# Performance work log

Hardware: AMD Instinct MI355X
Metric: run time of the kernel (lower is better)

Reference implementation:

```python
import jax, jax.numpy as jnp
import numpy as np

B, D, H, NL, NB = 131072, 64, 512, 3, 8
d = D // 2
EPS = 1e-5


def _mlp(x, W0, b0, Wh, bh, Wo, bo, act):
    # x: [B, d] -> [B, d]; hidden width H, NL hidden->hidden layers, linear output
    h = act(x @ W0 + b0)
    for i in range(Wh.shape[0]):
        h = act(h @ Wh[i] + bh[i])
    return h @ Wo + bo


def setup_inputs() -> dict:
    key = jax.random.key(0)
    ks = jax.random.split(key, 16)
    s = 0.05
    inp = {
        "y": jax.random.normal(ks[0], (B, D), dtype=jnp.float32),
        # s-network params, stacked over blocks
        "sW0": jax.random.normal(ks[1], (NB, d, H), dtype=jnp.float32) * s,
        "sb0": jnp.zeros((NB, H), jnp.float32),
        "sWh": jax.random.normal(ks[2], (NB, NL, H, H), dtype=jnp.float32) * s,
        "sbh": jnp.zeros((NB, NL, H), jnp.float32),
        "sWo": jax.random.normal(ks[3], (NB, H, d), dtype=jnp.float32) * s,
        "sbo": jnp.zeros((NB, d), jnp.float32),
        # t-network params
        "tW0": jax.random.normal(ks[4], (NB, d, H), dtype=jnp.float32) * s,
        "tb0": jnp.zeros((NB, H), jnp.float32),
        "tWh": jax.random.normal(ks[5], (NB, NL, H, H), dtype=jnp.float32) * s,
        "tbh": jnp.zeros((NB, NL, H), jnp.float32),
        "tWo": jax.random.normal(ks[6], (NB, H, d), dtype=jnp.float32) * s,
        "tbo": jnp.zeros((NB, d), jnp.float32),
        # BatchNorm flow params (log_gamma, beta init at 0 as in torch module)
        "bn_log_gamma": jnp.zeros((NB, D), jnp.float32),
        "bn_beta": jnp.zeros((NB, D), jnp.float32),
    }
    return inp


def reference(y, sW0, sb0, sWh, sbh, sWo, sbo,
              tW0, tb0, tWh, tbh, tWo, tbo,
              bn_log_gamma, bn_beta):
    act_s, act_t = jnp.tanh, jax.nn.relu
    log_det = jnp.zeros((y.shape[0], 1), y.dtype)
    for b in range(NB):
        # alternating slice/compliment: even blocks condition on first half
        if b % 2 == 0:
            ys, yc = y[:, :d], y[:, d:]
        else:
            ys, yc = y[:, d:], y[:, :d]
        s_out = _mlp(ys, sW0[b], sb0[b], sWh[b], sbh[b], sWo[b], sbo[b], act_s)
        t_out = _mlp(ys, tW0[b], tb0[b], tWh[b], tbh[b], tWo[b], tbo[b], act_t)
        zc = yc * jnp.exp(s_out) + t_out
        z = jnp.concatenate([ys, zc], axis=1) if b % 2 == 0 else jnp.concatenate([zc, ys], axis=1)
        log_det = log_det + jnp.sum(s_out, axis=1, keepdims=True)
        # Batch_Norm flow (training mode: batch stats, unbiased var like torch .var(0))
        mean = z.mean(axis=0)
        var = z.var(axis=0, ddof=1)
        x_hat = (z - mean) / jnp.sqrt(var + EPS)
        y = jnp.exp(bn_log_gamma[b]) * x_hat + bn_beta[b]
        log_det = log_det + jnp.sum(bn_log_gamma[b] - 0.5 * jnp.log(var + EPS))
    return y, log_det
```

## Files before the change

### kernel.cpp

```cpp
#include <hip/hip_runtime.h>

#define NBLK 8
#define BROWS 131072
#define HDIM 512
#define EPSV 1e-5f
#define WROWS 64

typedef __bf16 bf16x8 __attribute__((ext_vector_type(8)));
typedef __bf16 bf16x4 __attribute__((ext_vector_type(4)));
typedef float f32x4 __attribute__((ext_vector_type(4)));

#define PACK_NET 819200
#define PACK_H 16384
#define PACK_HEAD 802816

__device__ __forceinline__ float act_tanh_f(float x) {
  float e = __expf(x + x);
  return fmaf(-2.f, __builtin_amdgcn_rcpf(e + 1.f), 1.f);
}

template <int ACT>
__device__ __forceinline__ float apply_act(float v) {
  if (ACT == 1) return act_tanh_f(v);
  return fmaxf(v, 0.f);
}

template <int ACT>
__device__ __forceinline__ void dense_hidden(const __bf16* __restrict__ Wp,
                                             const float* __restrict__ bias,
                                             __bf16* hb, int w, int c,
                                             int quad, int lane) {
  f32x4 acc[4][4];
#pragma unroll
  for (int rb = 0; rb < 4; ++rb)
#pragma unroll
    for (int ft = 0; ft < 4; ++ft) acc[rb][ft] = (f32x4){0.f, 0.f, 0.f, 0.f};
  const __bf16* wp = Wp + (size_t)(w * 2) * 16384 + lane * 8;
  bf16x8 br[3][4];
#pragma unroll
  for (int s = 0; s < 2; ++s)
#pragma unroll
    for (int ft = 0; ft < 4; ++ft)
      br[s][ft] = *(const bf16x8*)(wp + (ft >> 1) * 16384 + (ft & 1) * 512 +
                                   s * 1024);
  const int msk = (c & 7) << 3;
  __builtin_amdgcn_s_setprio(1);
#pragma unroll
  for (int kt = 0; kt < 16; ++kt) {
    if (kt + 2 < 16) {
#pragma unroll
      for (int ft = 0; ft < 4; ++ft)
        br[(kt + 2) % 3][ft] = *(const bf16x8*)(wp + (ft >> 1) * 16384 +
                                                (ft & 1) * 512 + (kt + 2) * 1024);
    }
    const int sk = (kt * 32 + quad * 8) ^ msk;
#pragma unroll
    for (int rb = 0; rb < 4; ++rb) {
      bf16x8 hv = *(const bf16x8*)&hb[(rb * 16 + c) * HDIM + sk];
#pragma unroll
      for (int ft = 0; ft < 4; ++ft)
        acc[rb][ft] = __builtin_amdgcn_mfma_f32_16x16x32_bf16(br[kt % 3][ft], hv, acc[rb][ft], 0, 0, 0);
    }
  }
  __builtin_amdgcn_s_setprio(0);
  __syncthreads();
#pragma unroll
  for (int ft = 0; ft < 4; ++ft) {
    const f32x4 bi = *(const f32x4*)&bias[w * 64 + ft * 16 + quad * 4];
    const int fsw = (w * 64 + ft * 16 + quad * 4) ^ msk;
#pragma unroll
    for (int rb = 0; rb < 4; ++rb) {
      bf16x4 pk;
#pragma unroll
      for (int i = 0; i < 4; ++i)
        pk[i] = (__bf16)apply_act<ACT>(acc[rb][ft][i] + bi[i]);
      *(bf16x4*)&hb[(rb * 16 + c) * HDIM + fsw] = pk;
    }
  }
  __syncthreads();
}

template <int ACT>
__device__ __forceinline__ void dense_l0(const __bf16* __restrict__ pw,
                                         const float* __restrict__ b0,
                                         const __bf16* __restrict__ ys,
                                         __bf16* hb, int w, int c, int quad,
                                         int lane) {
  bf16x8 aw[4];
#pragma unroll
  for (int ft = 0; ft < 4; ++ft)
    aw[ft] = *(const bf16x8*)&pw[(size_t)(w * 2 + (ft >> 1)) * 1024 +
                                 (ft & 1) * 512 + lane * 8];
  f32x4 acc[4][4];
#pragma unroll
  for (int rb = 0; rb < 4; ++rb)
#pragma unroll
    for (int ft = 0; ft < 4; ++ft) acc[rb][ft] = (f32x4){0.f, 0.f, 0.f, 0.f};
  const int ysk = (quad * 8) ^ ((c & 3) << 3);
  __builtin_amdgcn_s_setprio(1);
#pragma unroll
  for (int rb = 0; rb < 4; ++rb) {
    bf16x8 yb = *(const bf16x8*)&ys[(rb * 16 + c) * 32 + ysk];
#pragma unroll
    for (int ft = 0; ft < 4; ++ft)
      acc[rb][ft] = __builtin_amdgcn_mfma_f32_16x16x32_bf16(aw[ft], yb, acc[rb][ft], 0, 0, 0);
  }
  __builtin_amdgcn_s_setprio(0);
  const int msk = (c & 7) << 3;
#pragma unroll
  for (int ft = 0; ft < 4; ++ft) {
    const f32x4 bi = *(const f32x4*)&b0[w * 64 + ft * 16 + quad * 4];
    const int fsw = (w * 64 + ft * 16 + quad * 4) ^ msk;
#pragma unroll
    for (int rb = 0; rb < 4; ++rb) {
      bf16x4 pk;
#pragma unroll
      for (int i = 0; i < 4; ++i)
        pk[i] = (__bf16)apply_act<ACT>(acc[rb][ft][i] + bi[i]);
      *(bf16x4*)&hb[(rb * 16 + c) * HDIM + fsw] = pk;
    }
  }
}

__device__ __forceinline__ f32x4 dense_head(const __bf16* __restrict__ ph,
                                            const float* __restrict__ bo,
                                            const __bf16* __restrict__ hb,
                                            int fb, int rb, int c, int quad,
                                            int lane) {
  const __bf16* wp = ph + (size_t)fb * 8192 + lane * 8;
  bf16x8 hr[3];
  hr[0] = *(const bf16x8*)wp;
  hr[1] = *(const bf16x8*)(wp + 512);
  f32x4 acc = (f32x4){0.f, 0.f, 0.f, 0.f};
  const int msk = (c & 7) << 3;
  __builtin_amdgcn_s_setprio(1);
#pragma unroll
  for (int kt = 0; kt < 16; ++kt) {
    if (kt + 2 < 16) hr[(kt + 2) % 3] = *(const bf16x8*)(wp + (kt + 2) * 512);
    bf16x8 hv = *(const bf16x8*)&hb[(rb * 16 + c) * HDIM + ((kt * 32 + quad * 8) ^ msk)];
    acc = __builtin_amdgcn_mfma_f32_16x16x32_bf16(hr[kt % 3], hv, acc, 0, 0, 0);
  }
  __builtin_amdgcn_s_setprio(0);
  const int f0 = fb * 16 + quad * 4;
  f32x4 bo4 = *(const f32x4*)&bo[f0];
#pragma unroll
  for (int i = 0; i < 4; ++i) acc[i] += bo4[i];
  return acc;
}

template <bool FIRST>
__global__ __launch_bounds__(512, 4) void fused_block(
    const float* __restrict__ src, const __bf16* __restrict__ pwS,
    const __bf16* __restrict__ pwT, const float* __restrict__ sb0,
    const float* __restrict__ sbh, const float* __restrict__ sbo,
    const float* __restrict__ tb0, const float* __restrict__ tbh,
    const float* __restrict__ tbo, const float* __restrict__ prevP,
    float* __restrict__ zbuf, float* __restrict__ ld,
    float* __restrict__ stats_out, int o) {
  __shared__ __bf16 hbuf[WROWS * HDIM];
  __shared__ __bf16 ysb[WROWS * 32];
  __shared__ float tout[WROWS * 36];
  const int tid = threadIdx.x;
  const int w = tid >> 6, lane = tid & 63, c = lane & 15, quad = lane >> 4;
  const size_t row0 = (size_t)blockIdx.x * WROWS;

  {
    const int row = tid >> 3, sub = tid & 7;
    const int col0 = o + sub * 4;
    f32x4 yv = *(const f32x4*)&src[(row0 + row) * 64 + col0];
    bf16x4 pv;
#pragma unroll
    for (int j = 0; j < 4; ++j) {
      const float A_ = FIRST ? 1.f : prevP[col0 + j];
      const float C_ = FIRST ? 0.f : prevP[64 + col0 + j];
      pv[j] = (__bf16)fmaf(A_, yv[j], C_);
    }
    *(bf16x4*)&ysb[row * 32 + ((sub * 4) ^ ((row & 3) << 3))] = pv;
  }
  __syncthreads();

  const int fb = w & 1, rb = w >> 1;
  const int f0 = fb * 16 + quad * 4;
  const int r = rb * 16 + c;

  dense_l0<2>(pwT, tb0, ysb, hbuf, w, c, quad, lane);
  __syncthreads();
  dense_hidden<2>(pwT + PACK_H, tbh, hbuf, w, c, quad, lane);
  dense_hidden<2>(pwT + PACK_H + 262144, tbh + 512, hbuf, w, c, quad, lane);
  dense_hidden<2>(pwT + PACK_H + 2 * 262144, tbh + 1024, hbuf, w, c, quad, lane);
  {
    f32x4 tvh = dense_head(pwT + PACK_HEAD, tbo, hbuf, fb, rb, c, quad, lane);
    *(f32x4*)&tout[r * 36 + f0] = tvh;
  }
  __syncthreads();

  dense_l0<1>(pwS, sb0, ysb, hbuf, w, c, quad, lane);
  __syncthreads();
  dense_hidden<1>(pwS + PACK_H, sbh, hbuf, w, c, quad, lane);
  dense_hidden<1>(pwS + PACK_H + 262144, sbh + 512, hbuf, w, c, quad, lane);
  dense_hidden<1>(pwS + PACK_H + 2 * 262144, sbh + 1024, hbuf, w, c, quad, lane);
  f32x4 sacc = dense_head(pwS + PACK_HEAD, sbo, hbuf, fb, rb, c, quad, lane);
  float sv[4];
#pragma unroll
  for (int i = 0; i < 4; ++i) sv[i] = sacc[i];

  const size_t grow = row0 + r;
  f32x4 tv = *(const f32x4*)&tout[r * 36 + f0];
  __syncthreads();
  float* cs = (float*)hbuf;
  float* lda = cs + 128;
  if (tid < 128) cs[tid] = 0.f;
  else if (tid < 192) lda[tid - 128] = 0.f;
  __syncthreads();

  const int oc = o ^ 32;
  float zc[4], yn2[4];
  {
    f32x4 pA1, pC1, pA2, pC2;
    if (FIRST) {
      pA1 = pA2 = (f32x4){1.f, 1.f, 1.f, 1.f};
      pC1 = pC2 = (f32x4){0.f, 0.f, 0.f, 0.f};
    } else {
      pA1 = *(const f32x4*)&prevP[oc + f0];
      pC1 = *(const f32x4*)&prevP[64 + oc + f0];
      pA2 = *(const f32x4*)&prevP[o + f0];
      pC2 = *(const f32x4*)&prevP[64 + o + f0];
    }
    f32x4 yv = *(const f32x4*)&src[grow * 64 + oc + f0];
    f32x4 zo;
#pragma unroll
    for (int i = 0; i < 4; ++i) {
      zc[i] = fmaf(fmaf(pA1[i], yv[i], pC1[i]), __expf(sv[i]), tv[i]);
      zo[i] = zc[i];
    }
    *(f32x4*)&zbuf[grow * 64 + oc + f0] = zo;
    f32x4 yv2 = *(const f32x4*)&src[grow * 64 + o + f0];
    f32x4 yo;
#pragma unroll
    for (int i = 0; i < 4; ++i) {
      yn2[i] = fmaf(pA2[i], yv2[i], pC2[i]);
      yo[i] = yn2[i];
    }
    *(f32x4*)&zbuf[grow * 64 + o + f0] = yo;
  }

  {
    float ssum = sv[0] + sv[1] + sv[2] + sv[3];
    ssum += __shfl_xor(ssum, 16);
    ssum += __shfl_xor(ssum, 32);
    if (quad == 0) atomicAdd(&lda[r], ssum);
  }

#pragma unroll
  for (int i = 0; i < 4; ++i) {
    float v = zc[i], q = zc[i] * zc[i];
    float v2 = yn2[i], q2 = yn2[i] * yn2[i];
#pragma unroll
    for (int m = 1; m < 16; m <<= 1) {
      v += __shfl_xor(v, m);  q += __shfl_xor(q, m);
      v2 += __shfl_xor(v2, m); q2 += __shfl_xor(q2, m);
    }
    if (c == 0) {
      atomicAdd(&cs[oc + f0 + i], v);
      atomicAdd(&cs[64 + oc + f0 + i], q);
      atomicAdd(&cs[o + f0 + i], v2);
      atomicAdd(&cs[64 + o + f0 + i], q2);
    }
  }
  __syncthreads();
  if (tid < 128) {
    atomicAdd(&stats_out[tid], cs[tid]);
  } else if (tid < 192) {
    const int rr = tid - 128;
    const size_t gr = row0 + rr;
    if (FIRST) ld[gr] = lda[rr]; else ld[gr] += lda[rr];
  }
}


__global__ void stats_kernel(const float* __restrict__ raw,
                             const float* __restrict__ lg,
                             const float* __restrict__ beta,
                             float* __restrict__ param,
                             float* __restrict__ ld_scalar) {
  const int t = threadIdx.x;
  const float S = raw[t], SS = raw[64 + t];
  const float mean = S / (float)BROWS;
  const float var = (SS - S * mean) / (float)(BROWS - 1);
  const float inv = rsqrtf(var + EPSV);
  const float g = __expf(lg[t]);
  const float A = g * inv;
  param[t] = A;
  param[64 + t] = beta[t] - mean * A;
  float contrib = lg[t] - 0.5f * __logf(var + EPSV);
  contrib += __shfl_xor(contrib, 1);  contrib += __shfl_xor(contrib, 2);
  contrib += __shfl_xor(contrib, 4);  contrib += __shfl_xor(contrib, 8);
  contrib += __shfl_xor(contrib, 16); contrib += __shfl_xor(contrib, 32);
  if (t == 0) atomicAdd(ld_scalar, contrib);
}

__global__ void final_kernel(float* __restrict__ out,
                             const float* __restrict__ param7,
                             const float* __restrict__ ld_scalar) {
  const size_t gid = (size_t)blockIdx.x * 256 + threadIdx.x;
  const size_t total = (size_t)BROWS * 64;
  const int col = gid & 63;
  const float z = out[gid];
  out[gid] = param7[col] * z + param7[64 + col];
  if (gid < BROWS) out[total + gid] += ld_scalar[0];
}

__global__ void pack_weights(const float* __restrict__ sW0,
                             const float* __restrict__ sWh,
                             const float* __restrict__ sWo,
                             const float* __restrict__ tW0,
                             const float* __restrict__ tWh,
                             const float* __restrict__ tWo,
                             __bf16* __restrict__ dst) {
  const int gid = blockIdx.x * 256 + threadIdx.x;
  const int gpn = PACK_NET / 8;
  const int b = gid / (2 * gpn);
  const int rr0 = gid % (2 * gpn);
  const int net = rr0 / gpn;
  const size_t o = (size_t)(rr0 % gpn) * 8;
  const float* W0 = net ? tW0 : sW0;
  const float* Wh = net ? tWh : sWh;
  const float* Wo = net ? tWo : sWo;
  __bf16* d = dst + ((size_t)b * 2 + net) * PACK_NET + o;
  float v[8];
  if (o < PACK_H) {
    const int idx = (int)(o >> 3);
    const int lane = idx & 63, fbb = (idx >> 6) & 1, w = (idx >> 7) & 15;
    const int cc = lane & 15, q = lane >> 4;
    const int f = w * 32 + fbb * 16 + cc;
    const float* s = W0 + (size_t)b * 32 * 512;
#pragma unroll
    for (int j = 0; j < 8; ++j) v[j] = s[(size_t)(q * 8 + j) * 512 + f];
  } else if (o < PACK_HEAD) {
    const size_t oo = o - PACK_H;
    const int l = (int)(oo >> 18);
    const int idx = (int)((oo & 262143) >> 3);
    const int lane = idx & 63, fbb = (idx >> 6) & 1, kt = (idx >> 7) & 15,
              w = (idx >> 11) & 15;
    const int cc = lane & 15, q = lane >> 4;
    const int f = w * 32 + fbb * 16 + cc;
    const float* s = Wh + ((size_t)(b * 3 + l)) * 512 * 512;
#pragma unroll
    for (int j = 0; j < 8; ++j) v[j] = s[(size_t)(kt * 32 + q * 8 + j) * 512 + f];
  } else {
    const size_t oo = o - PACK_HEAD;
    const int idx = (int)(oo >> 3);
    const int lane = idx & 63, kt = (idx >> 6) & 15, fbb = (idx >> 10) & 1;
    const int cc = lane & 15, q = lane >> 4;
    const int f = fbb * 16 + cc;
    const float* s = Wo + (size_t)b * 512 * 32;
#pragma unroll
    for (int j = 0; j < 8; ++j) v[j] = s[(size_t)(kt * 32 + q * 8 + j) * 32 + f];
  }
  bf16x8 pv;
#pragma unroll
  for (int j = 0; j < 8; ++j) pv[j] = (__bf16)v[j];
  *(bf16x8*)d = pv;
}


extern "C" void kernel_launch(void* const* d_in, const int* in_sizes, int n_in,
                              void* d_out, int out_size, void* d_ws, size_t ws_size,
                              hipStream_t stream) {
  const float* y_in = (const float*)d_in[0];
  const float* sW0 = (const float*)d_in[1];
  const float* sb0 = (const float*)d_in[2];
  const float* sWh = (const float*)d_in[3];
  const float* sbh = (const float*)d_in[4];
  const float* sWo = (const float*)d_in[5];
  const float* sbo = (const float*)d_in[6];
  const float* tW0 = (const float*)d_in[7];
  const float* tb0 = (const float*)d_in[8];
  const float* tWh = (const float*)d_in[9];
  const float* tbh = (const float*)d_in[10];
  const float* tWo = (const float*)d_in[11];
  const float* tbo = (const float*)d_in[12];
  const float* bn_lg = (const float*)d_in[13];
  const float* bn_bt = (const float*)d_in[14];

  char* p = (char*)d_ws;
  __bf16* packed = (__bf16*)p; p += (size_t)NBLK * 2 * PACK_NET * 2;
  float* stats_raw = (float*)p; p += NBLK * 128 * 4;
  float* ld_scalar = (float*)p; p += 256;
  float* stats_param = (float*)p; p += NBLK * 128 * 4;

  float* out = (float*)d_out;
  float* zbuf = out;
  float* ld = out + (size_t)BROWS * 64;

  pack_weights<<<(NBLK * 2 * PACK_NET / 8) / 256, 256, 0, stream>>>(
      sW0, sWh, sWo, tW0, tWh, tWo, packed);
  hipMemsetAsync(stats_raw, 0, NBLK * 128 * 4 + 256, stream);

  const int GG = BROWS / WROWS;

  for (int b = 0; b < NBLK; ++b) {
    const int o = (b & 1) ? 32 : 0;
    const __bf16* pwS = packed + (size_t)b * 2 * PACK_NET;
    const __bf16* pwT = pwS + PACK_NET;
    float* praw = stats_raw + b * 128;
    const float* srcb = (b == 0) ? y_in : zbuf;

    if (b == 0) {
      fused_block<true><<<GG, 512, 0, stream>>>(srcb, pwS, pwT,
          sb0, sbh, sbo, tb0, tbh, tbo, nullptr, zbuf, ld, praw, o);
    } else {
      fused_block<false><<<GG, 512, 0, stream>>>(srcb, pwS, pwT,
          sb0 + b * 512, sbh + (size_t)b * 1536, sbo + b * 32,
          tb0 + b * 512, tbh + (size_t)b * 1536, tbo + b * 32,
          stats_param + (size_t)(b - 1) * 128, zbuf, ld, praw, o);
    }
    stats_kernel<<<1, 64, 0, stream>>>(praw, bn_lg + b * 64, bn_bt + b * 64,
                                       stats_param + (size_t)b * 128, ld_scalar);
  }

  final_kernel<<<(BROWS * 64) / 256, 256, 0, stream>>>(
      out, stats_param + 7 * 128, ld_scalar);
}
```

Before: 3.913 ms.

## Reorder hidden weight pack k-major and alternate s/t net order per block

Measured after the change: 3.991 ms. No clear change (+2.0%).

```diff
diff --git a/kernel.cpp b/kernel.cpp
--- a/kernel.cpp
+++ b/kernel.cpp
@@ -19,44 +19,37 @@
   return fmaf(-2.f, __builtin_amdgcn_rcpf(e + 1.f), 1.f);
 }
 
-template <int ACT>
-__device__ __forceinline__ float apply_act(float v) {
-  if (ACT == 1) return act_tanh_f(v);
-  return fmaxf(v, 0.f);
-}
-
-template <int ACT>
 __device__ __forceinline__ void dense_hidden(const __bf16* __restrict__ Wp,
                                              const float* __restrict__ bias,
-                                             __bf16* hb, int w, int c,
+                                             __bf16* hb, int act, int w, int c,
                                              int quad, int lane) {
   f32x4 acc[4][4];
 #pragma unroll
   for (int rb = 0; rb < 4; ++rb)
 #pragma unroll
     for (int ft = 0; ft < 4; ++ft) acc[rb][ft] = (f32x4){0.f, 0.f, 0.f, 0.f};
-  const __bf16* wp = Wp + (size_t)(w * 2) * 16384 + lane * 8;
+  const __bf16* wp = Wp + (size_t)w * 2048 + lane * 8;
   bf16x8 br[3][4];
 #pragma unroll
   for (int s = 0; s < 2; ++s)
 #pragma unroll
     for (int ft = 0; ft < 4; ++ft)
-      br[s][ft] = *(const bf16x8*)(wp + (ft >> 1) * 16384 + (ft & 1) * 512 +
-                                   s * 1024);
+      br[s][ft] = *(const bf16x8*)(wp + s * 16384 + ft * 512);
   const int msk = (c & 7) << 3;
+  const int rowb = c << 9;
+  const int qb = quad << 3;
   __builtin_amdgcn_s_setprio(1);
 #pragma unroll
   for (int kt = 0; kt < 16; ++kt) {
     if (kt + 2 < 16) {
 #pragma unroll
       for (int ft = 0; ft < 4; ++ft)
-        br[(kt + 2) % 3][ft] = *(const bf16x8*)(wp + (ft >> 1) * 16384 +
-                                                (ft & 1) * 512 + (kt + 2) * 1024);
-    }
-    const int sk = (kt * 32 + quad * 8) ^ msk;
+        br[(kt + 2) % 3][ft] = *(const bf16x8*)(wp + (kt + 2) * 16384 + ft * 512);
+    }
+    const int sk = (((kt * 32 + qb) ^ msk) + rowb);
 #pragma unroll
     for (int rb = 0; rb < 4; ++rb) {
-      bf16x8 hv = *(const bf16x8*)&hb[(rb * 16 + c) * HDIM + sk];
+      bf16x8 hv = *(const bf16x8*)&hb[sk + rb * 8192];
 #pragma unroll
       for (int ft = 0; ft < 4; ++ft)
         acc[rb][ft] = __builtin_amdgcn_mfma_f32_16x16x32_bf16(br[kt % 3][ft], hv, acc[rb][ft], 0, 0, 0);
@@ -64,33 +57,48 @@
   }
   __builtin_amdgcn_s_setprio(0);
   __syncthreads();
-#pragma unroll
-  for (int ft = 0; ft < 4; ++ft) {
-    const f32x4 bi = *(const f32x4*)&bias[w * 64 + ft * 16 + quad * 4];
-    const int fsw = (w * 64 + ft * 16 + quad * 4) ^ msk;
-#pragma unroll
-    for (int rb = 0; rb < 4; ++rb) {
-      bf16x4 pk;
-#pragma unroll
-      for (int i = 0; i < 4; ++i)
-        pk[i] = (__bf16)apply_act<ACT>(acc[rb][ft][i] + bi[i]);
-      *(bf16x4*)&hb[(rb * 16 + c) * HDIM + fsw] = pk;
-    }
-  }
-  __syncthreads();
-}
-
-template <int ACT>
+  const int wq = w * 64 + quad * 4;
+  if (act == 1) {
+#pragma unroll
+    for (int ft = 0; ft < 4; ++ft) {
+      const f32x4 bi = *(const f32x4*)&bias[wq + ft * 16];
+      const int fsw = ((wq + ft * 16) ^ msk) + rowb;
+#pragma unroll
+      for (int rb = 0; rb < 4; ++rb) {
+        bf16x4 pk;
+#pragma unroll
+        for (int i = 0; i < 4; ++i)
+          pk[i] = (__bf16)act_tanh_f(acc[rb][ft][i] + bi[i]);
+        *(bf16x4*)&hb[fsw + rb * 8192] = pk;
+      }
+    }
+  } else {
+#pragma unroll
+    for (int ft = 0; ft < 4; ++ft) {
+      const f32x4 bi = *(const f32x4*)&bias[wq + ft * 16];
+      const int fsw = ((wq + ft * 16) ^ msk) + rowb;
+#pragma unroll
+      for (int rb = 0; rb < 4; ++rb) {
+        bf16x4 pk;
+#pragma unroll
+        for (int i = 0; i < 4; ++i)
+          pk[i] = (__bf16)fmaxf(acc[rb][ft][i] + bi[i], 0.f);
+        *(bf16x4*)&hb[fsw + rb * 8192] = pk;
+      }
+    }
+  }
+  __syncthreads();
+}
+
 __device__ __forceinline__ void dense_l0(const __bf16* __restrict__ pw,
                                          const float* __restrict__ b0,
                                          const __bf16* __restrict__ ys,
-                                         __bf16* hb, int w, int c, int quad,
-                                         int lane) {
+                                         __bf16* hb, int act, int w, int c,
+                                         int quad, int lane) {
   bf16x8 aw[4];
 #pragma unroll
   for (int ft = 0; ft < 4; ++ft)
-    aw[ft] = *(const bf16x8*)&pw[(size_t)(w * 2 + (ft >> 1)) * 1024 +
-                                 (ft & 1) * 512 + lane * 8];
+    aw[ft] = *(const bf16x8*)&pw[(size_t)w * 2048 + ft * 512 + lane * 8];
   f32x4 acc[4][4];
 #pragma unroll
   for (int rb = 0; rb < 4; ++rb)
@@ -107,17 +115,35 @@
   }
   __builtin_amdgcn_s_setprio(0);
   const int msk = (c & 7) << 3;
-#pragma unroll
-  for (int ft = 0; ft < 4; ++ft) {
-    const f32x4 bi = *(const f32x4*)&b0[w * 64 + ft * 16 + quad * 4];
-    const int fsw = (w * 64 + ft * 16 + quad * 4) ^ msk;
-#pragma unroll
-    for (int rb = 0; rb < 4; ++rb) {
-      bf16x4 pk;
-#pragma unroll
-      for (int i = 0; i < 4; ++i)
-        pk[i] = (__bf16)apply_act<ACT>(acc[rb][ft][i] + bi[i]);
-      *(bf16x4*)&hb[(rb * 16 + c) * HDIM + fsw] = pk;
+  const int rowb = c << 9;
+  const int wq = w * 64 + quad * 4;
+  if (act == 1) {
+#pragma unroll
+    for (int ft = 0; ft < 4; ++ft) {
+      const f32x4 bi = *(const f32x4*)&b0[wq + ft * 16];
+      const int fsw = ((wq + ft * 16) ^ msk) + rowb;
+#pragma unroll
+      for (int rb = 0; rb < 4; ++rb) {
+        bf16x4 pk;
+#pragma unroll
+        for (int i = 0; i < 4; ++i)
+          pk[i] = (__bf16)act_tanh_f(acc[rb][ft][i] + bi[i]);
+        *(bf16x4*)&hb[fsw + rb * 8192] = pk;
+      }
+    }
+  } else {
+#pragma unroll
+    for (int ft = 0; ft < 4; ++ft) {
+      const f32x4 bi = *(const f32x4*)&b0[wq + ft * 16];
+      const int fsw = ((wq + ft * 16) ^ msk) + rowb;
+#pragma unroll
+      for (int rb = 0; rb < 4; ++rb) {
+        bf16x4 pk;
+#pragma unroll
+        for (int i = 0; i < 4; ++i)
+          pk[i] = (__bf16)fmaxf(acc[rb][ft][i] + bi[i], 0.f);
+        *(bf16x4*)&hb[fsw + rb * 8192] = pk;
+      }
     }
   }
 }
@@ -146,6 +172,21 @@
 #pragma unroll
   for (int i = 0; i < 4; ++i) acc[i] += bo4[i];
   return acc;
+}
+
+__device__ __forceinline__ f32x4 run_net(const __bf16* __restrict__ pw,
+                                         const float* __restrict__ b0,
+                                         const float* __restrict__ bh,
+                                         const float* __restrict__ bo, int act,
+                                         const __bf16* __restrict__ ysb,
+                                         __bf16* hbuf, int w, int fb, int rb,
+                                         int c, int quad, int lane) {
+  dense_l0(pw, b0, ysb, hbuf, act, w, c, quad, lane);
+  __syncthreads();
+  dense_hidden(pw + PACK_H, bh, hbuf, act, w, c, quad, lane);
+  dense_hidden(pw + PACK_H + 262144, bh + 512, hbuf, act, w, c, quad, lane);
+  dense_hidden(pw + PACK_H + 2 * 262144, bh + 1024, hbuf, act, w, c, quad, lane);
+  return dense_head(pw + PACK_HEAD, bo, hbuf, fb, rb, c, quad, lane);
 }
 
 template <bool FIRST>
@@ -183,29 +224,30 @@
   const int f0 = fb * 16 + quad * 4;
   const int r = rb * 16 + c;
 
-  dense_l0<2>(pwT, tb0, ysb, hbuf, w, c, quad, lane);
-  __syncthreads();
-  dense_hidden<2>(pwT + PACK_H, tbh, hbuf, w, c, quad, lane);
-  dense_hidden<2>(pwT + PACK_H + 262144, tbh + 512, hbuf, w, c, quad, lane);
-  dense_hidden<2>(pwT + PACK_H + 2 * 262144, tbh + 1024, hbuf, w, c, quad, lane);
+  const int par = (blockIdx.x >> 8) & 1;
+  const __bf16* pwA = par ? pwS : pwT;
+  const __bf16* pwB = par ? pwT : pwS;
+  const float* b0A = par ? sb0 : tb0;  const float* b0B = par ? tb0 : sb0;
+  const float* bhA = par ? sbh : tbh;  const float* bhB = par ? tbh : sbh;
+  const float* boA = par ? sbo : tbo;  const float* boB = par ? tbo : sbo;
+  const int actA = par ? 1 : 2, actB = par ? 2 : 1;
+
   {
-    f32x4 tvh = dense_head(pwT + PACK_HEAD, tbo, hbuf, fb, rb, c, quad, lane);
-    *(f32x4*)&tout[r * 36 + f0] = tvh;
-  }
-  __syncthreads();
-
-  dense_l0<1>(pwS, sb0, ysb, hbuf, w, c, quad, lane);
-  __syncthreads();
-  dense_hidden<1>(pwS + PACK_H, sbh, hbuf, w, c, quad, lane);
-  dense_hidden<1>(pwS + PACK_H + 262144, sbh + 512, hbuf, w, c, quad, lane);
-  dense_hidden<1>(pwS + PACK_H + 2 * 262144, sbh + 1024, hbuf, w, c, quad, lane);
-  f32x4 sacc = dense_head(pwS + PACK_HEAD, sbo, hbuf, fb, rb, c, quad, lane);
+    f32x4 hA = run_net(pwA, b0A, bhA, boA, actA, ysb, hbuf, w, fb, rb, c, quad, lane);
+    *(f32x4*)&tout[r * 36 + f0] = hA;
+  }
+  __syncthreads();
+
+  f32x4 hB = run_net(pwB, b0B, bhB, boB, actB, ysb, hbuf, w, fb, rb, c, quad, lane);
+
+  f32x4 stash = *(const f32x4*)&tout[r * 36 + f0];
+  f32x4 tv = par ? hB : stash;
+  f32x4 svv = par ? stash : hB;
   float sv[4];
 #pragma unroll
-  for (int i = 0; i < 4; ++i) sv[i] = sacc[i];
+  for (int i = 0; i < 4; ++i) sv[i] = svv[i];
 
   const size_t grow = row0 + r;
-  f32x4 tv = *(const f32x4*)&tout[r * 36 + f0];
   __syncthreads();
   float* cs = (float*)hbuf;
   float* lda = cs + 128;
@@ -340,10 +382,9 @@
     const size_t oo = o - PACK_H;
     const int l = (int)(oo >> 18);
     const int idx = (int)((oo & 262143) >> 3);
-    const int lane = idx & 63, fbb = (idx >> 6) & 1, kt = (idx >> 7) & 15,
-              w = (idx >> 11) & 15;
+    const int lane = idx & 63, T = (idx >> 6) & 31, kt = (idx >> 11) & 15;
     const int cc = lane & 15, q = lane >> 4;
-    const int f = w * 32 + fbb * 16 + cc;
+    const int f = T * 16 + cc;
     const float* s = Wh + ((size_t)(b * 3 + l)) * 512 * 512;
 #pragma unroll
     for (int j = 0; j < 8; ++j) v[j] = s[(size_t)(kt * 32 + q * 8 + j) * 512 + f];
```

## Switch hidden layers to 32x32x16 MFMA with repacked weight layout

Applied to the files above, without the earlier changes.

Measured after the change: 4.322 ms. 10.4% more time.

```diff
diff --git a/kernel.cpp b/kernel.cpp
--- a/kernel.cpp
+++ b/kernel.cpp
@@ -9,6 +9,7 @@
 typedef __bf16 bf16x8 __attribute__((ext_vector_type(8)));
 typedef __bf16 bf16x4 __attribute__((ext_vector_type(4)));
 typedef float f32x4 __attribute__((ext_vector_type(4)));
+typedef float f32x16 __attribute__((ext_vector_type(16)));
 
 #define PACK_NET 819200
 #define PACK_H 16384
@@ -28,55 +29,58 @@
 template <int ACT>
 __device__ __forceinline__ void dense_hidden(const __bf16* __restrict__ Wp,
                                              const float* __restrict__ bias,
-                                             __bf16* hb, int w, int c,
-                                             int quad, int lane) {
-  f32x4 acc[4][4];
-#pragma unroll
-  for (int rb = 0; rb < 4; ++rb)
-#pragma unroll
-    for (int ft = 0; ft < 4; ++ft) acc[rb][ft] = (f32x4){0.f, 0.f, 0.f, 0.f};
-  const __bf16* wp = Wp + (size_t)(w * 2) * 16384 + lane * 8;
-  bf16x8 br[3][4];
-#pragma unroll
-  for (int s = 0; s < 2; ++s)
-#pragma unroll
-    for (int ft = 0; ft < 4; ++ft)
-      br[s][ft] = *(const bf16x8*)(wp + (ft >> 1) * 16384 + (ft & 1) * 512 +
-                                   s * 1024);
-  const int msk = (c & 7) << 3;
+                                             __bf16* hb, int w, int lane) {
+  f32x16 acc[2][2];
+#pragma unroll
+  for (int F = 0; F < 2; ++F)
+#pragma unroll
+    for (int R = 0; R < 2; ++R)
+#pragma unroll
+      for (int i = 0; i < 16; ++i) acc[F][R][i] = 0.f;
+  const __bf16* wp = Wp + (size_t)w * 1024 + lane * 8;
+  const int row = lane & 31;
+  const int hi5 = lane >> 5;
+  const int swz = (row & 7) << 3;
+  const int rb0 = row * HDIM;
+  bf16x8 aA[3][2];
+#pragma unroll
+  for (int s = 0; s < 2; ++s) {
+    aA[s][0] = *(const bf16x8*)(wp + s * 8192);
+    aA[s][1] = *(const bf16x8*)(wp + s * 8192 + 512);
+  }
   __builtin_amdgcn_s_setprio(1);
 #pragma unroll
-  for (int kt = 0; kt < 16; ++kt) {
-    if (kt + 2 < 16) {
-#pragma unroll
-      for (int ft = 0; ft < 4; ++ft)
-        br[(kt + 2) % 3][ft] = *(const bf16x8*)(wp + (ft >> 1) * 16384 +
-                                                (ft & 1) * 512 + (kt + 2) * 1024);
-    }
-    const int sk = (kt * 32 + quad * 8) ^ msk;
-#pragma unroll
-    for (int rb = 0; rb < 4; ++rb) {
-      bf16x8 hv = *(const bf16x8*)&hb[(rb * 16 + c) * HDIM + sk];
-#pragma unroll
-      for (int ft = 0; ft < 4; ++ft)
-        acc[rb][ft] = __builtin_amdgcn_mfma_f32_16x16x32_bf16(br[kt % 3][ft], hv, acc[rb][ft], 0, 0, 0);
-    }
+  for (int kt = 0; kt < 32; ++kt) {
+    if (kt + 2 < 32) {
+      aA[(kt + 2) % 3][0] = *(const bf16x8*)(wp + (kt + 2) * 8192);
+      aA[(kt + 2) % 3][1] = *(const bf16x8*)(wp + (kt + 2) * 8192 + 512);
+    }
+    const int sk = (kt * 16 + hi5 * 8) ^ swz;
+    bf16x8 b0 = *(const bf16x8*)&hb[rb0 + sk];
+    bf16x8 b1 = *(const bf16x8*)&hb[rb0 + 32 * HDIM + sk];
+    acc[0][0] = __builtin_amdgcn_mfma_f32_32x32x16_bf16(aA[kt % 3][0], b0, acc[0][0], 0, 0, 0);
+    acc[1][0] = __builtin_amdgcn_mfma_f32_32x32x16_bf16(aA[kt % 3][1], b0, acc[1][0], 0, 0, 0);
+    acc[0][1] = __builtin_amdgcn_mfma_f32_32x32x16_bf16(aA[kt % 3][0], b1, acc[0][1], 0, 0, 0);
+    acc[1][1] = __builtin_amdgcn_mfma_f32_32x32x16_bf16(aA[kt % 3][1], b1, acc[1][1], 0, 0, 0);
   }
   __builtin_amdgcn_s_setprio(0);
   __syncthreads();
 #pragma unroll
-  for (int ft = 0; ft < 4; ++ft) {
-    const f32x4 bi = *(const f32x4*)&bias[w * 64 + ft * 16 + quad * 4];
-    const int fsw = (w * 64 + ft * 16 + quad * 4) ^ msk;
-#pragma unroll
-    for (int rb = 0; rb < 4; ++rb) {
-      bf16x4 pk;
-#pragma unroll
-      for (int i = 0; i < 4; ++i)
-        pk[i] = (__bf16)apply_act<ACT>(acc[rb][ft][i] + bi[i]);
-      *(bf16x4*)&hb[(rb * 16 + c) * HDIM + fsw] = pk;
-    }
-  }
+  for (int F = 0; F < 2; ++F)
+#pragma unroll
+    for (int g = 0; g < 4; ++g) {
+      const int f0 = w * 64 + F * 32 + g * 8 + hi5 * 4;
+      const f32x4 bi = *(const f32x4*)&bias[f0];
+      const int st = f0 ^ swz;
+#pragma unroll
+      for (int R = 0; R < 2; ++R) {
+        bf16x4 pk;
+#pragma unroll
+        for (int i = 0; i < 4; ++i)
+          pk[i] = (__bf16)apply_act<ACT>(acc[F][R][g * 4 + i] + bi[i]);
+        *(bf16x4*)&hb[(R * 32 + row) * HDIM + st] = pk;
+      }
+    }
   __syncthreads();
 }
 
@@ -89,8 +93,7 @@
   bf16x8 aw[4];
 #pragma unroll
   for (int ft = 0; ft < 4; ++ft)
-    aw[ft] = *(const bf16x8*)&pw[(size_t)(w * 2 + (ft >> 1)) * 1024 +
-                                 (ft & 1) * 512 + lane * 8];
+    aw[ft] = *(const bf16x8*)&pw[(size_t)w * 2048 + ft * 512 + lane * 8];
   f32x4 acc[4][4];
 #pragma unroll
   for (int rb = 0; rb < 4; ++rb)
@@ -107,17 +110,19 @@
   }
   __builtin_amdgcn_s_setprio(0);
   const int msk = (c & 7) << 3;
+  const int rowb = c << 9;
+  const int wq = w * 64 + quad * 4;
 #pragma unroll
   for (int ft = 0; ft < 4; ++ft) {
-    const f32x4 bi = *(const f32x4*)&b0[w * 64 + ft * 16 + quad * 4];
-    const int fsw = (w * 64 + ft * 16 + quad * 4) ^ msk;
+    const f32x4 bi = *(const f32x4*)&b0[wq + ft * 16];
+    const int fsw = ((wq + ft * 16) ^ msk) + rowb;
 #pragma unroll
     for (int rb = 0; rb < 4; ++rb) {
       bf16x4 pk;
 #pragma unroll
       for (int i = 0; i < 4; ++i)
         pk[i] = (__bf16)apply_act<ACT>(acc[rb][ft][i] + bi[i]);
-      *(bf16x4*)&hb[(rb * 16 + c) * HDIM + fsw] = pk;
+      *(bf16x4*)&hb[fsw + rb * 8192] = pk;
     }
   }
 }
@@ -148,6 +153,22 @@
   return acc;
 }
 
+template <int ACT>
+__device__ __forceinline__ f32x4 run_net(const __bf16* __restrict__ pw,
+                                         const float* __restrict__ b0,
+                                         const float* __restrict__ bh,
+                                         const float* __restrict__ bo,
+                                         const __bf16* __restrict__ ysb,
+                                         __bf16* hbuf, int w, int fb, int rb,
+                                         int c, int quad, int lane) {
+  dense_l0<ACT>(pw, b0, ysb, hbuf, w, c, quad, lane);
+  __syncthreads();
+  dense_hidden<ACT>(pw + PACK_H, bh, hbuf, w, lane);
+  dense_hidden<ACT>(pw + PACK_H + 262144, bh + 512, hbuf, w, lane);
+  dense_hidden<ACT>(pw + PACK_H + 2 * 262144, bh + 1024, hbuf, w, lane);
+  return dense_head(pw + PACK_HEAD, bo, hbuf, fb, rb, c, quad, lane);
+}
+
 template <bool FIRST>
 __global__ __launch_bounds__(512, 4) void fused_block(
     const float* __restrict__ src, const __bf16* __restrict__ pwS,
@@ -159,7 +180,6 @@
     float* __restrict__ stats_out, int o) {
   __shared__ __bf16 hbuf[WROWS * HDIM];
   __shared__ __bf16 ysb[WROWS * 32];
-  __shared__ float tout[WROWS * 36];
   const int tid = threadIdx.x;
   const int w = tid >> 6, lane = tid & 63, c = lane & 15, quad = lane >> 4;
   const size_t row0 = (size_t)blockIdx.x * WROWS;
@@ -183,29 +203,15 @@
   const int f0 = fb * 16 + quad * 4;
   const int r = rb * 16 + c;
 
-  dense_l0<2>(pwT, tb0, ysb, hbuf, w, c, quad, lane);
-  __syncthreads();
-  dense_hidden<2>(pwT + PACK_H, tbh, hbuf, w, c, quad, lane);
-  dense_hidden<2>(pwT + PACK_H + 262144, tbh + 512, hbuf, w, c, quad, lane);
-  dense_hidden<2>(pwT + PACK_H + 2 * 262144, tbh + 1024, hbuf, w, c, quad, lane);
-  {
-    f32x4 tvh = dense_head(pwT + PACK_HEAD, tbo, hbuf, fb, rb, c, quad, lane);
-    *(f32x4*)&tout[r * 36 + f0] = tvh;
-  }
-  __syncthreads();
-
-  dense_l0<1>(pwS, sb0, ysb, hbuf, w, c, quad, lane);
-  __syncthreads();
-  dense_hidden<1>(pwS + PACK_H, sbh, hbuf, w, c, quad, lane);
-  dense_hidden<1>(pwS + PACK_H + 262144, sbh + 512, hbuf, w, c, quad, lane);
-  dense_hidden<1>(pwS + PACK_H + 2 * 262144, sbh + 1024, hbuf, w, c, quad, lane);
-  f32x4 sacc = dense_head(pwS + PACK_HEAD, sbo, hbuf, fb, rb, c, quad, lane);
+  f32x4 tv = run_net<2>(pwT, tb0, tbh, tbo, ysb, hbuf, w, fb, rb, c, quad, lane);
+  __syncthreads();
+
+  f32x4 sacc = run_net<1>(pwS, sb0, sbh, sbo, ysb, hbuf, w, fb, rb, c, quad, lane);
   float sv[4];
 #pragma unroll
   for (int i = 0; i < 4; ++i) sv[i] = sacc[i];
 
   const size_t grow = row0 + r;
-  f32x4 tv = *(const f32x4*)&tout[r * 36 + f0];
   __syncthreads();
   float* cs = (float*)hbuf;
   float* lda = cs + 128;
@@ -340,13 +346,12 @@
     const size_t oo = o - PACK_H;
     const int l = (int)(oo >> 18);
     const int idx = (int)((oo & 262143) >> 3);
-    const int lane = idx & 63, fbb = (idx >> 6) & 1, kt = (idx >> 7) & 15,
-              w = (idx >> 11) & 15;
-    const int cc = lane & 15, q = lane >> 4;
-    const int f = w * 32 + fbb * 16 + cc;
+    const int lane = idx & 63, T = (idx >> 6) & 15, kt = (idx >> 10) & 31;
+    const int f = T * 32 + (lane & 31);
+    const int k0 = kt * 16 + (lane >> 5) * 8;
     const float* s = Wh + ((size_t)(b * 3 + l)) * 512 * 512;
 #pragma unroll
-    for (int j = 0; j < 8; ++j) v[j] = s[(size_t)(kt * 32 + q * 8 + j) * 512 + f];
+    for (int j = 0; j < 8; ++j) v[j] = s[(size_t)(k0 + j) * 512 + f];
   } else {
     const size_t oo = o - PACK_HEAD;
     const int idx = (int)(oo >> 3);
```

## Chain weight prefetch across hidden layers and keep t-output in registers

Applied to the files above, without the earlier changes.

Result: no change. 3.985 ms (+1.8%).

```diff
diff --git a/kernel.cpp b/kernel.cpp
--- a/kernel.cpp
+++ b/kernel.cpp
@@ -25,33 +25,34 @@
   return fmaxf(v, 0.f);
 }
 
-template <int ACT>
+template <int ACT, int PHASE, bool CHAIN>
 __device__ __forceinline__ void dense_hidden(const __bf16* __restrict__ Wp,
+                                             const __bf16* __restrict__ Wn,
                                              const float* __restrict__ bias,
-                                             __bf16* hb, int w, int c,
-                                             int quad, int lane) {
+                                             __bf16* hb, bf16x8 (&br)[3][4],
+                                             int w, int c, int quad, int lane) {
   f32x4 acc[4][4];
 #pragma unroll
   for (int rb = 0; rb < 4; ++rb)
 #pragma unroll
     for (int ft = 0; ft < 4; ++ft) acc[rb][ft] = (f32x4){0.f, 0.f, 0.f, 0.f};
   const __bf16* wp = Wp + (size_t)(w * 2) * 16384 + lane * 8;
-  bf16x8 br[3][4];
-#pragma unroll
-  for (int s = 0; s < 2; ++s)
-#pragma unroll
-    for (int ft = 0; ft < 4; ++ft)
-      br[s][ft] = *(const bf16x8*)(wp + (ft >> 1) * 16384 + (ft & 1) * 512 +
-                                   s * 1024);
+  const __bf16* wn = Wn + (size_t)(w * 2) * 16384 + lane * 8;
   const int msk = (c & 7) << 3;
   __builtin_amdgcn_s_setprio(1);
 #pragma unroll
   for (int kt = 0; kt < 16; ++kt) {
-    if (kt + 2 < 16) {
+    const int pf = kt + 2;
+    if (pf < 16) {
 #pragma unroll
       for (int ft = 0; ft < 4; ++ft)
-        br[(kt + 2) % 3][ft] = *(const bf16x8*)(wp + (ft >> 1) * 16384 +
-                                                (ft & 1) * 512 + (kt + 2) * 1024);
+        br[(pf + PHASE) % 3][ft] = *(const bf16x8*)(wp + (ft >> 1) * 16384 +
+                                                    (ft & 1) * 512 + pf * 1024);
+    } else if (CHAIN) {
+#pragma unroll
+      for (int ft = 0; ft < 4; ++ft)
+        br[(pf + PHASE) % 3][ft] = *(const bf16x8*)(wn + (ft >> 1) * 16384 +
+                                                    (ft & 1) * 512 + (pf - 16) * 1024);
     }
     const int sk = (kt * 32 + quad * 8) ^ msk;
 #pragma unroll
@@ -59,7 +60,7 @@
       bf16x8 hv = *(const bf16x8*)&hb[(rb * 16 + c) * HDIM + sk];
 #pragma unroll
       for (int ft = 0; ft < 4; ++ft)
-        acc[rb][ft] = __builtin_amdgcn_mfma_f32_16x16x32_bf16(br[kt % 3][ft], hv, acc[rb][ft], 0, 0, 0);
+        acc[rb][ft] = __builtin_amdgcn_mfma_f32_16x16x32_bf16(br[(kt + PHASE) % 3][ft], hv, acc[rb][ft], 0, 0, 0);
     }
   }
   __builtin_amdgcn_s_setprio(0);
@@ -107,17 +108,19 @@
   }
   __builtin_amdgcn_s_setprio(0);
   const int msk = (c & 7) << 3;
+  const int rowb = c << 9;
+  const int wq = w * 64 + quad * 4;
 #pragma unroll
   for (int ft = 0; ft < 4; ++ft) {
-    const f32x4 bi = *(const f32x4*)&b0[w * 64 + ft * 16 + quad * 4];
-    const int fsw = (w * 64 + ft * 16 + quad * 4) ^ msk;
+    const f32x4 bi = *(const f32x4*)&b0[wq + ft * 16];
+    const int fsw = ((wq + ft * 16) ^ msk) + rowb;
 #pragma unroll
     for (int rb = 0; rb < 4; ++rb) {
       bf16x4 pk;
 #pragma unroll
       for (int i = 0; i < 4; ++i)
         pk[i] = (__bf16)apply_act<ACT>(acc[rb][ft][i] + bi[i]);
-      *(bf16x4*)&hb[(rb * 16 + c) * HDIM + fsw] = pk;
+      *(bf16x4*)&hb[fsw + rb * 8192] = pk;
     }
   }
 }
@@ -148,6 +151,35 @@
   return acc;
 }
 
+template <int ACT>
+__device__ __forceinline__ f32x4 run_net(const __bf16* __restrict__ pw,
+                                         const float* __restrict__ b0,
+                                         const float* __restrict__ bh,
+                                         const float* __restrict__ bo,
+                                         const __bf16* __restrict__ ysb,
+                                         __bf16* hbuf, int w, int fb, int rb,
+                                         int c, int quad, int lane) {
+  const __bf16* W1 = pw + PACK_H;
+  const __bf16* W2 = pw + PACK_H + 262144;
+  const __bf16* W3 = pw + PACK_H + 2 * 262144;
+  dense_l0<ACT>(pw, b0, ysb, hbuf, w, c, quad, lane);
+  bf16x8 br[3][4];
+  {
+    const __bf16* wp1 = W1 + (size_t)(w * 2) * 16384 + lane * 8;
+#pragma unroll
+    for (int s = 0; s < 2; ++s)
+#pragma unroll
+      for (int ft = 0; ft < 4; ++ft)
+        br[s][ft] = *(const bf16x8*)(wp1 + (ft >> 1) * 16384 + (ft & 1) * 512 +
+                                     s * 1024);
+  }
+  __syncthreads();
+  dense_hidden<ACT, 0, true>(W1, W2, bh, hbuf, br, w, c, quad, lane);
+  dense_hidden<ACT, 1, true>(W2, W3, bh + 512, hbuf, br, w, c, quad, lane);
+  dense_hidden<ACT, 2, false>(W3, W3, bh + 1024, hbuf, br, w, c, quad, lane);
+  return dense_head(pw + PACK_HEAD, bo, hbuf, fb, rb, c, quad, lane);
+}
+
 template <bool FIRST>
 __global__ __launch_bounds__(512, 4) void fused_block(
     const float* __restrict__ src, const __bf16* __restrict__ pwS,
@@ -159,7 +191,6 @@
     float* __restrict__ stats_out, int o) {
   __shared__ __bf16 hbuf[WROWS * HDIM];
   __shared__ __bf16 ysb[WROWS * 32];
-  __shared__ float tout[WROWS * 36];
   const int tid = threadIdx.x;
   const int w = tid >> 6, lane = tid & 63, c = lane & 15, quad = lane >> 4;
   const size_t row0 = (size_t)blockIdx.x * WROWS;
@@ -183,29 +214,15 @@
   const int f0 = fb * 16 + quad * 4;
   const int r = rb * 16 + c;
 
-  dense_l0<2>(pwT, tb0, ysb, hbuf, w, c, quad, lane);
-  __syncthreads();
-  dense_hidden<2>(pwT + PACK_H, tbh, hbuf, w, c, quad, lane);
-  dense_hidden<2>(pwT + PACK_H + 262144, tbh + 512, hbuf, w, c, quad, lane);
-  dense_hidden<2>(pwT + PACK_H + 2 * 262144, tbh + 1024, hbuf, w, c, quad, lane);
-  {
-    f32x4 tvh = dense_head(pwT + PACK_HEAD, tbo, hbuf, fb, rb, c, quad, lane);
-    *(f32x4*)&tout[r * 36 + f0] = tvh;
-  }
-  __syncthreads();
-
-  dense_l0<1>(pwS, sb0, ysb, hbuf, w, c, quad, lane);
-  __syncthreads();
-  dense_hidden<1>(pwS + PACK_H, sbh, hbuf, w, c, quad, lane);
-  dense_hidden<1>(pwS + PACK_H + 262144, sbh + 512, hbuf, w, c, quad, lane);
-  dense_hidden<1>(pwS + PACK_H + 2 * 262144, sbh + 1024, hbuf, w, c, quad, lane);
-  f32x4 sacc = dense_head(pwS + PACK_HEAD, sbo, hbuf, fb, rb, c, quad, lane);
+  f32x4 tv = run_net<2>(pwT, tb0, tbh, tbo, ysb, hbuf, w, fb, rb, c, quad, lane);
+  __syncthreads();
+
+  f32x4 sacc = run_net<1>(pwS, sb0, sbh, sbo, ysb, hbuf, w, fb, rb, c, quad, lane);
   float sv[4];
 #pragma unroll
   for (int i = 0; i < 4; ++i) sv[i] = sacc[i];
 
   const size_t grow = row0 + r;
-  f32x4 tv = *(const f32x4*)&tout[r * 36 + f0];
   __syncthreads();
   float* cs = (float*)hbuf;
   float* lda = cs + 128;
```
